# Performance work log

Measured on AMD Instinct MI355X. Metric: run time of the kernel, lower is better.

## Reference

```python
import jax, jax.numpy as jnp
import numpy as np

N = 2048          # target nodes
N_NODES = 2048    # neighbor pool
D_IN = 256
D_EDGE = 16
D_HID = 32
D_OUT = 256


def _mlp(h, w1, b1, w2, b2):
    # Linear -> Tanh -> Linear
    return jnp.tanh(h @ w1 + b1) @ w2 + b2


def setup_inputs() -> dict:
    key = jax.random.key(0)
    ks = jax.random.split(key, 20)
    s = 0.05
    inp = {
        "x": jax.random.normal(ks[0], (N, D_IN), jnp.float32),
        "neibs": jax.random.normal(ks[1], (N_NODES, D_IN), jnp.float32),
        "edge_emb": jax.random.normal(ks[2], (N * N_NODES, D_EDGE), jnp.float32),
        # multiplicative binary mask (float, as in original ws * mask)
        "mask": (jax.random.uniform(ks[3], (N, N_NODES)) < 0.7).astype(jnp.float32),
        "ax_w1": jax.random.normal(ks[4], (D_IN, D_HID), jnp.float32) * s,
        "ax_b1": jnp.zeros((D_HID,), jnp.float32),
        "ax_w2": jax.random.normal(ks[5], (D_HID, D_HID), jnp.float32) * s,
        "ax_b2": jnp.zeros((D_HID,), jnp.float32),
        "an_w1": jax.random.normal(ks[6], (D_IN, D_HID), jnp.float32) * s,
        "an_b1": jnp.zeros((D_HID,), jnp.float32),
        "an_w2": jax.random.normal(ks[7], (D_HID, D_HID), jnp.float32) * s,
        "an_b2": jnp.zeros((D_HID,), jnp.float32),
        "ae_w1": jax.random.normal(ks[8], (D_EDGE, D_HID), jnp.float32) * s,
        "ae_b1": jnp.zeros((D_HID,), jnp.float32),
        "ae_w2": jax.random.normal(ks[9], (D_HID, D_HID), jnp.float32) * s,
        "ae_b2": jnp.zeros((D_HID,), jnp.float32),
        "fcx_w": jax.random.normal(ks[10], (2 * D_IN, D_OUT), jnp.float32) * s,
        "fcx_b": jnp.zeros((D_OUT,), jnp.float32),
    }
    return inp


def reference(x, neibs, edge_emb, mask,
              ax_w1, ax_b1, ax_w2, ax_b2,
              an_w1, an_b1, an_w2, an_b2,
              ae_w1, ae_b1, ae_w2, ae_b2,
              fcx_w, fcx_b):
    x_att = _mlp(x, ax_w1, ax_b1, ax_w2, ax_b2)          # (N, H)
    neib_att = _mlp(neibs, an_w1, an_b1, an_w2, an_b2)   # (n_nodes, H)
    # edge attention is computed in the original forward but never used (dead code)
    _edge_att = _mlp(edge_emb, ae_w1, ae_b1, ae_w2, ae_b2)
    # multiplicative masking (NOT additive -inf), then softmax over neighbors
    ws = jnp.einsum('nh,mh->nm', x_att, neib_att) * mask  # (N, n_nodes)
    ws = jax.nn.softmax(ws, axis=1)
    agg_neib = jax.nn.sigmoid(ws @ neibs)                 # (N, D_IN)
    # concat_node=False path: concat -> fc_x -> sigmoid; dropout is identity (eval)
    out = jax.nn.sigmoid(jnp.concatenate([x, agg_neib], axis=1) @ fcx_w + fcx_b)
    return out
```

## Files before the change

kernel.cpp:

```cpp
#include <hip/hip_runtime.h>
#include <hip/hip_bf16.h>
#include <math.h>

#define NROWS 2048
#define DIN 256
#define DH 32
#define DOUT 256

typedef unsigned short ushort_t;
typedef unsigned int uint_t;
typedef __attribute__((ext_vector_type(8))) short short8;
typedef __attribute__((ext_vector_type(4))) float floatx4;

__device__ __forceinline__ float bf2f(uint_t u) {
    union { uint_t i; float f; } v; v.i = u << 16; return v.f;
}
__device__ __forceinline__ ushort_t f2bf(float f) {
    __hip_bfloat16 h = __float2bfloat16(f);
    union { __hip_bfloat16 h; ushort_t u; } v; v.h = h; return v.u;
}
__device__ __forceinline__ float sigm(float v) { return 1.0f / (1.0f + __expf(-v)); }

#define PSTR 2072
#define ASTR 536

__global__ __launch_bounds__(256) void prep_kernel(
    const float* __restrict__ x, const float* __restrict__ neibs,
    const float* __restrict__ ax_w1, const float* __restrict__ ax_b1,
    const float* __restrict__ ax_w2, const float* __restrict__ ax_b2,
    const float* __restrict__ an_w1, const float* __restrict__ an_b1,
    const float* __restrict__ an_w2, const float* __restrict__ an_b2,
    const float* __restrict__ fcx_w,
    float* __restrict__ x_att, ushort_t* __restrict__ n_att,
    short8* __restrict__ B_pack, short8* __restrict__ W_pack)
{
    const int t = threadIdx.x;
    const int b = blockIdx.x;

    __shared__ float srow[8][DIN];
    __shared__ float hbuf[8][DH];

    if (b < 512) {
        const bool is_x = b < 256;
        const int row0 = (is_x ? b : b - 256) * 8;
        const float* __restrict__ in = is_x ? x : neibs;
        const float* __restrict__ w1 = is_x ? ax_w1 : an_w1;
        const float* __restrict__ b1 = is_x ? ax_b1 : an_b1;
        const float* __restrict__ w2 = is_x ? ax_w2 : an_w2;
        const float* __restrict__ b2 = is_x ? ax_b2 : an_b2;

        const int r = t >> 5, c = t & 31;
        {
            const float4* in4 = (const float4*)(in + (row0 + r) * DIN);
            float4 a = in4[c * 2], bb = in4[c * 2 + 1];
            *(float4*)&srow[r][c * 8] = a;
            *(float4*)&srow[r][c * 8 + 4] = bb;
        }
        __syncthreads();

        float s = b1[c];
#pragma unroll 8
        for (int k = 0; k < DIN; ++k) s += srow[r][k] * w1[k * DH + c];
        s = tanhf(s);
        hbuf[r][c] = s;
        __syncthreads();

        float s2 = b2[c];
#pragma unroll
        for (int j = 0; j < DH; ++j) s2 += hbuf[r][j] * w2[j * DH + c];

        if (is_x) x_att[(row0 + r) * DH + c] = s2;
        else      n_att[(row0 + r) * DH + c] = f2bf(s2);
    } else if (b < 768) {
        const int g = (b - 512) * 256 + t;
        const int n = g & 15, q = (g >> 4) & 3, tt = (g >> 6) & 3, w = (g >> 8) & 3;
        const int s = g >> 10;
        const int ncol = w * 64 + tt * 16 + n;
        const int kb = 32 * s + 8 * q;
        short8 v;
#pragma unroll
        for (int j = 0; j < 8; ++j)
            v[j] = (short)f2bf(neibs[(size_t)(kb + j) * DIN + ncol]);
        B_pack[g] = v;
    } else {
        const int g = (b - 768) * 256 + t;
        const int n = g & 15, q = (g >> 4) & 3, tt = (g >> 6) & 3, w = (g >> 8) & 3;
        const int s = g >> 10;
        const int ncol = w * 64 + tt * 16 + n;
        const int kb = 32 * s + 8 * q;
        short8 v;
#pragma unroll
        for (int j = 0; j < 8; ++j)
            v[j] = (short)f2bf(fcx_w[(size_t)(kb + j) * DOUT + ncol]);
        W_pack[g] = v;
    }
}

__global__ __launch_bounds__(256) void attn_kernel(
    const float* __restrict__ x, const float* __restrict__ mask,
    const float* __restrict__ x_att, const ushort_t* __restrict__ n_att,
    const short8* __restrict__ B_pack, const short8* __restrict__ W_pack,
    const float* __restrict__ fcx_b, float* __restrict__ out)
{
    __shared__ __align__(16) ushort_t pTr[8 * PSTR];
    __shared__ __align__(16) ushort_t ATr[8 * ASTR];
    __shared__ float row_inv[8];

    const int t = threadIdx.x;
    const int n0 = blockIdx.x * 8;
    const int wv = t >> 6, lane = t & 63;

#pragma unroll
    for (int r = 0; r < 8; ++r)
        ATr[r * ASTR + t] = f2bf(x[(size_t)(n0 + r) * DIN + t]);

    const int r0 = 2 * wv, r1 = r0 + 1;
    float xa0[DH], xa1[DH];
#pragma unroll
    for (int h = 0; h < DH; ++h) {
        xa0[h] = x_att[(n0 + r0) * DH + h];
        xa1[h] = x_att[(n0 + r1) * DH + h];
    }
    float mx0 = -1e30f, mx1 = -1e30f;
    const uint4* na4 = (const uint4*)n_att;
    for (int it = 0; it < 32; ++it) {
        const int m = it * 64 + lane;
        float s0 = 0.f, s1 = 0.f;
#pragma unroll
        for (int qq = 0; qq < 4; ++qq) {
            uint4 v = na4[m * 4 + qq];
            uint_t wsw[4] = { v.x, v.y, v.z, v.w };
#pragma unroll
            for (int u = 0; u < 4; ++u) {
                const float f0 = bf2f(wsw[u] & 0xffffu);
                const float f1 = bf2f(wsw[u] >> 16);
                const int h = qq * 8 + u * 2;
                s0 += xa0[h] * f0;     s1 += xa1[h] * f0;
                s0 += xa0[h + 1] * f1; s1 += xa1[h + 1] * f1;
            }
        }
        s0 *= mask[(size_t)(n0 + r0) * NROWS + m];
        s1 *= mask[(size_t)(n0 + r1) * NROWS + m];
        mx0 = fmaxf(mx0, s0); mx1 = fmaxf(mx1, s1);
        pTr[r0 * PSTR + m] = f2bf(s0);
        pTr[r1 * PSTR + m] = f2bf(s1);
    }
#pragma unroll
    for (int off = 32; off >= 1; off >>= 1) {
        mx0 = fmaxf(mx0, __shfl_xor(mx0, off));
        mx1 = fmaxf(mx1, __shfl_xor(mx1, off));
    }
    float l0 = 0.f, l1 = 0.f;
    for (int it = 0; it < 32; ++it) {
        const int m = it * 64 + lane;
        const float e0 = __expf(bf2f(pTr[r0 * PSTR + m]) - mx0);
        const float e1 = __expf(bf2f(pTr[r1 * PSTR + m]) - mx1);
        l0 += e0; l1 += e1;
        pTr[r0 * PSTR + m] = f2bf(e0);
        pTr[r1 * PSTR + m] = f2bf(e1);
    }
#pragma unroll
    for (int off = 32; off >= 1; off >>= 1) {
        l0 += __shfl_xor(l0, off);
        l1 += __shfl_xor(l1, off);
    }
    if (lane == 0) { row_inv[r0] = 1.f / l0; row_inv[r1] = 1.f / l1; }
    __syncthreads();

    const int q = lane >> 4;
    const int ar = lane & 7;
    const char* aBase = (const char*)pTr + ar * (PSTR * 2) + q * 16;

    floatx4 acc[4];
#pragma unroll
    for (int tt = 0; tt < 4; ++tt) acc[tt] = (floatx4){0.f, 0.f, 0.f, 0.f};

    for (int s = 0; s < 64; ++s) {
        const short8 av = *(const short8*)(aBase + s * 64);
#pragma unroll
        for (int tt = 0; tt < 4; ++tt) {
            const int slab = (s * 4 + wv) * 4 + tt;
            const short8 bv = B_pack[slab * 64 + lane];
            acc[tt] = __builtin_amdgcn_mfma_f32_16x16x32_bf16(av, bv, acc[tt], 0, 0, 0);
        }
    }
    if (lane < 32) {
        const int col = lane & 15;
        const int rbase = (lane >> 4) * 4;
#pragma unroll
        for (int tt = 0; tt < 4; ++tt) {
            const int n = wv * 64 + tt * 16 + col;
#pragma unroll
            for (int rg = 0; rg < 4; ++rg) {
                const int row = rbase + rg;
                ATr[row * ASTR + 256 + n] = f2bf(sigm(acc[tt][rg] * row_inv[row]));
            }
        }
    }
    __syncthreads();

    floatx4 acc2[4];
#pragma unroll
    for (int tt = 0; tt < 4; ++tt) acc2[tt] = (floatx4){0.f, 0.f, 0.f, 0.f};

    const char* a2Base = (const char*)ATr + ar * (ASTR * 2) + q * 16;
    for (int s = 0; s < 16; ++s) {
        const short8 av = *(const short8*)(a2Base + s * 64);
#pragma unroll
        for (int tt = 0; tt < 4; ++tt) {
            const int slab = (s * 4 + wv) * 4 + tt;
            const short8 bv = W_pack[slab * 64 + lane];
            acc2[tt] = __builtin_amdgcn_mfma_f32_16x16x32_bf16(av, bv, acc2[tt], 0, 0, 0);
        }
    }
    if (lane < 32) {
        const int col = lane & 15;
        const int rbase = (lane >> 4) * 4;
#pragma unroll
        for (int tt = 0; tt < 4; ++tt) {
            const int n = wv * 64 + tt * 16 + col;
            const float bias = fcx_b[n];
#pragma unroll
            for (int rg = 0; rg < 4; ++rg) {
                const int row = rbase + rg;
                out[(size_t)(n0 + row) * DOUT + n] = sigm(acc2[tt][rg] + bias);
            }
        }
    }
}

extern "C" void kernel_launch(void* const* d_in, const int* in_sizes, int n_in,
                              void* d_out, int out_size, void* d_ws, size_t ws_size,
                              hipStream_t stream) {
    const float* x      = (const float*)d_in[0];
    const float* neibs  = (const float*)d_in[1];
    const float* mask   = (const float*)d_in[3];
    const float* ax_w1  = (const float*)d_in[4];
    const float* ax_b1  = (const float*)d_in[5];
    const float* ax_w2  = (const float*)d_in[6];
    const float* ax_b2  = (const float*)d_in[7];
    const float* an_w1  = (const float*)d_in[8];
    const float* an_b1  = (const float*)d_in[9];
    const float* an_w2  = (const float*)d_in[10];
    const float* an_b2  = (const float*)d_in[11];
    const float* fcx_w  = (const float*)d_in[16];
    const float* fcx_b  = (const float*)d_in[17];
    float* out = (float*)d_out;

    char* ws = (char*)d_ws;
    float*    x_att  = (float*)ws;
    ushort_t* n_att  = (ushort_t*)(ws + 262144);
    short8*   B_pack = (short8*)(ws + 393216);
    short8*   W_pack = (short8*)(ws + 1441792);

    prep_kernel<<<832, 256, 0, stream>>>(
        x, neibs, ax_w1, ax_b1, ax_w2, ax_b2,
        an_w1, an_b1, an_w2, an_b2, fcx_w,
        x_att, n_att, B_pack, W_pack);

    attn_kernel<<<256, 256, 0, stream>>>(
        x, mask, x_att, n_att, B_pack, W_pack, fcx_b, out);
}
```

Baseline: 411.0 us.

## Use MFMA for attention scores, split-K with 8 waves, LDS-tiled weight packing

The attention-score dot products move from scalar FMAs over bf16-unpacked vectors to MFMA 16x16x32 on prepacked bf16 x_att and n_att fragments. The attention kernel doubles to 512 threads (8 waves), splitting K across two wave groups for both GEMMs with an LDS reduction, and softmax becomes one wave per row with a register-held pass. Prep packing now stages neibs and fcx_w tiles in LDS for coalesced reads and uses fewer blocks. Costs are extra syncs and LDS reduction traffic, and x_att is now rounded to bf16, which lowers the precision of the scores.

Result: faster. 384.1 us (-6.5%).

```diff
diff --git a/kernel.cpp b/kernel.cpp
--- a/kernel.cpp
+++ b/kernel.cpp
@@ -21,8 +21,8 @@
 }
 __device__ __forceinline__ float sigm(float v) { return 1.0f / (1.0f + __expf(-v)); }
 
-#define PSTR 2072
-#define ASTR 536
+#define PSTR 2056
+#define ASTR 520
 
 __global__ __launch_bounds__(256) void prep_kernel(
     const float* __restrict__ x, const float* __restrict__ neibs,
@@ -31,16 +31,18 @@
     const float* __restrict__ an_w1, const float* __restrict__ an_b1,
     const float* __restrict__ an_w2, const float* __restrict__ an_b2,
     const float* __restrict__ fcx_w,
-    float* __restrict__ x_att, ushort_t* __restrict__ n_att,
+    ushort_t* __restrict__ x_attB, short8* __restrict__ n_attP,
     short8* __restrict__ B_pack, short8* __restrict__ W_pack)
 {
+    __shared__ float smem[32 * 256];
     const int t = threadIdx.x;
     const int b = blockIdx.x;
 
-    __shared__ float srow[8][DIN];
-    __shared__ float hbuf[8][DH];
-
     if (b < 512) {
+        float (*srow)[DIN] = (float (*)[DIN])smem;
+        float* hbuf = smem + 8 * DIN;
+        float* sbuf = smem + 8 * DIN + 8 * DH;
+
         const bool is_x = b < 256;
         const int row0 = (is_x ? b : b - 256) * 8;
         const float* __restrict__ in = is_x ? x : neibs;
@@ -51,7 +53,7 @@
 
         const int r = t >> 5, c = t & 31;
         {
-            const float4* in4 = (const float4*)(in + (row0 + r) * DIN);
+            const float4* in4 = (const float4*)(in + (size_t)(row0 + r) * DIN);
             float4 a = in4[c * 2], bb = in4[c * 2 + 1];
             *(float4*)&srow[r][c * 8] = a;
             *(float4*)&srow[r][c * 8 + 4] = bb;
@@ -62,43 +64,75 @@
 #pragma unroll 8
         for (int k = 0; k < DIN; ++k) s += srow[r][k] * w1[k * DH + c];
         s = tanhf(s);
-        hbuf[r][c] = s;
+        hbuf[r * DH + c] = s;
         __syncthreads();
 
         float s2 = b2[c];
 #pragma unroll
-        for (int j = 0; j < DH; ++j) s2 += hbuf[r][j] * w2[j * DH + c];
-
-        if (is_x) x_att[(row0 + r) * DH + c] = s2;
-        else      n_att[(row0 + r) * DH + c] = f2bf(s2);
-    } else if (b < 768) {
-        const int g = (b - 512) * 256 + t;
-        const int n = g & 15, q = (g >> 4) & 3, tt = (g >> 6) & 3, w = (g >> 8) & 3;
-        const int s = g >> 10;
-        const int ncol = w * 64 + tt * 16 + n;
-        const int kb = 32 * s + 8 * q;
-        short8 v;
-#pragma unroll
-        for (int j = 0; j < 8; ++j)
-            v[j] = (short)f2bf(neibs[(size_t)(kb + j) * DIN + ncol]);
-        B_pack[g] = v;
+        for (int j = 0; j < DH; ++j) s2 += hbuf[r * DH + j] * w2[j * DH + c];
+
+        if (is_x) {
+            x_attB[(size_t)(row0 + r) * DH + c] = f2bf(s2);
+        } else {
+            sbuf[r * DH + c] = s2;
+            __syncthreads();
+            if (t < 32) {
+                const int r2 = t >> 2, q = t & 3;
+                const int row = row0 + r2;
+                short8 v;
+#pragma unroll
+                for (int j = 0; j < 8; ++j) v[j] = (short)f2bf(sbuf[r2 * DH + q * 8 + j]);
+                n_attP[(row >> 4) * 64 + q * 16 + (row & 15)] = v;
+            }
+        }
+    } else if (b < 576) {
+        const int s = b - 512;
+        float* tile = smem;
+#pragma unroll
+        for (int i = 0; i < 8; ++i) {
+            const int e = i * 256 + t;
+            const int row = e >> 6, c4 = e & 63;
+            const float4 v = ((const float4*)neibs)[(size_t)(32 * s + row) * 64 + c4];
+            *(float4*)&tile[row * 256 + c4 * 4] = v;
+        }
+        __syncthreads();
+#pragma unroll
+        for (int i = 0; i < 4; ++i) {
+            const int G = i * 256 + t;
+            const int n = G & 15, q = (G >> 4) & 3, tt = (G >> 6) & 3, w = G >> 8;
+            const int col = w * 64 + tt * 16 + n;
+            short8 v;
+#pragma unroll
+            for (int j = 0; j < 8; ++j) v[j] = (short)f2bf(tile[(8 * q + j) * 256 + col]);
+            B_pack[s * 1024 + G] = v;
+        }
     } else {
-        const int g = (b - 768) * 256 + t;
-        const int n = g & 15, q = (g >> 4) & 3, tt = (g >> 6) & 3, w = (g >> 8) & 3;
-        const int s = g >> 10;
-        const int ncol = w * 64 + tt * 16 + n;
-        const int kb = 32 * s + 8 * q;
-        short8 v;
-#pragma unroll
-        for (int j = 0; j < 8; ++j)
-            v[j] = (short)f2bf(fcx_w[(size_t)(kb + j) * DOUT + ncol]);
-        W_pack[g] = v;
-    }
-}
-
-__global__ __launch_bounds__(256) void attn_kernel(
+        const int s = b - 576;
+        float* tile = smem;
+#pragma unroll
+        for (int i = 0; i < 8; ++i) {
+            const int e = i * 256 + t;
+            const int row = e >> 6, c4 = e & 63;
+            const float4 v = ((const float4*)fcx_w)[(size_t)(32 * s + row) * 64 + c4];
+            *(float4*)&tile[row * 256 + c4 * 4] = v;
+        }
+        __syncthreads();
+#pragma unroll
+        for (int i = 0; i < 4; ++i) {
+            const int G = i * 256 + t;
+            const int n = G & 15, q = (G >> 4) & 3, tt = (G >> 6) & 3, w = G >> 8;
+            const int col = w * 64 + tt * 16 + n;
+            short8 v;
+#pragma unroll
+            for (int j = 0; j < 8; ++j) v[j] = (short)f2bf(tile[(8 * q + j) * 256 + col]);
+            W_pack[s * 1024 + G] = v;
+        }
+    }
+}
+
+__global__ __launch_bounds__(512, 2) void attn_kernel(
     const float* __restrict__ x, const float* __restrict__ mask,
-    const float* __restrict__ x_att, const ushort_t* __restrict__ n_att,
+    const ushort_t* __restrict__ x_attB, const short8* __restrict__ n_attP,
     const short8* __restrict__ B_pack, const short8* __restrict__ W_pack,
     const float* __restrict__ fcx_b, float* __restrict__ out)
 {
@@ -108,122 +142,145 @@
 
     const int t = threadIdx.x;
     const int n0 = blockIdx.x * 8;
-    const int wv = t >> 6, lane = t & 63;
-
-#pragma unroll
-    for (int r = 0; r < 8; ++r)
-        ATr[r * ASTR + t] = f2bf(x[(size_t)(n0 + r) * DIN + t]);
-
-    const int r0 = 2 * wv, r1 = r0 + 1;
-    float xa0[DH], xa1[DH];
-#pragma unroll
-    for (int h = 0; h < DH; ++h) {
-        xa0[h] = x_att[(n0 + r0) * DH + h];
-        xa1[h] = x_att[(n0 + r1) * DH + h];
-    }
-    float mx0 = -1e30f, mx1 = -1e30f;
-    const uint4* na4 = (const uint4*)n_att;
-    for (int it = 0; it < 32; ++it) {
-        const int m = it * 64 + lane;
-        float s0 = 0.f, s1 = 0.f;
-#pragma unroll
-        for (int qq = 0; qq < 4; ++qq) {
-            uint4 v = na4[m * 4 + qq];
-            uint_t wsw[4] = { v.x, v.y, v.z, v.w };
-#pragma unroll
-            for (int u = 0; u < 4; ++u) {
-                const float f0 = bf2f(wsw[u] & 0xffffu);
-                const float f1 = bf2f(wsw[u] >> 16);
-                const int h = qq * 8 + u * 2;
-                s0 += xa0[h] * f0;     s1 += xa1[h] * f0;
-                s0 += xa0[h + 1] * f1; s1 += xa1[h + 1] * f1;
-            }
-        }
-        s0 *= mask[(size_t)(n0 + r0) * NROWS + m];
-        s1 *= mask[(size_t)(n0 + r1) * NROWS + m];
-        mx0 = fmaxf(mx0, s0); mx1 = fmaxf(mx1, s1);
-        pTr[r0 * PSTR + m] = f2bf(s0);
-        pTr[r1 * PSTR + m] = f2bf(s1);
-    }
-#pragma unroll
-    for (int off = 32; off >= 1; off >>= 1) {
-        mx0 = fmaxf(mx0, __shfl_xor(mx0, off));
-        mx1 = fmaxf(mx1, __shfl_xor(mx1, off));
-    }
-    float l0 = 0.f, l1 = 0.f;
-    for (int it = 0; it < 32; ++it) {
-        const int m = it * 64 + lane;
-        const float e0 = __expf(bf2f(pTr[r0 * PSTR + m]) - mx0);
-        const float e1 = __expf(bf2f(pTr[r1 * PSTR + m]) - mx1);
-        l0 += e0; l1 += e1;
-        pTr[r0 * PSTR + m] = f2bf(e0);
-        pTr[r1 * PSTR + m] = f2bf(e1);
-    }
-#pragma unroll
-    for (int off = 32; off >= 1; off >>= 1) {
-        l0 += __shfl_xor(l0, off);
-        l1 += __shfl_xor(l1, off);
-    }
-    if (lane == 0) { row_inv[r0] = 1.f / l0; row_inv[r1] = 1.f / l1; }
-    __syncthreads();
-
-    const int q = lane >> 4;
-    const int ar = lane & 7;
-    const char* aBase = (const char*)pTr + ar * (PSTR * 2) + q * 16;
-
-    floatx4 acc[4];
-#pragma unroll
-    for (int tt = 0; tt < 4; ++tt) acc[tt] = (floatx4){0.f, 0.f, 0.f, 0.f};
-
-    for (int s = 0; s < 64; ++s) {
-        const short8 av = *(const short8*)(aBase + s * 64);
-#pragma unroll
-        for (int tt = 0; tt < 4; ++tt) {
-            const int slab = (s * 4 + wv) * 4 + tt;
-            const short8 bv = B_pack[slab * 64 + lane];
-            acc[tt] = __builtin_amdgcn_mfma_f32_16x16x32_bf16(av, bv, acc[tt], 0, 0, 0);
-        }
-    }
-    if (lane < 32) {
-        const int col = lane & 15;
-        const int rbase = (lane >> 4) * 4;
-#pragma unroll
-        for (int tt = 0; tt < 4; ++tt) {
-            const int n = wv * 64 + tt * 16 + col;
+    const int w = t >> 6, lane = t & 63;
+    const int q = lane >> 4, nn = lane & 15;
+    const int arow = lane & 7;
+    const int rbase = (lane >> 4) * 4;
+
+#pragma unroll
+    for (int i = 0; i < 4; ++i) {
+        const int e = i * 512 + t;
+        const int r = e >> 8, k = e & 255;
+        ATr[r * ASTR + k] = f2bf(x[(size_t)(n0 + r) * DIN + k]);
+    }
+
+    const short8 av_s = *(const short8*)(x_attB + (size_t)(n0 + arow) * DH + q * 8);
+#pragma unroll 4
+    for (int i = 0; i < 16; ++i) {
+        const int tl = w * 16 + i;
+        const short8 bv = n_attP[tl * 64 + lane];
+        floatx4 c = __builtin_amdgcn_mfma_f32_16x16x32_bf16(
+            av_s, bv, (floatx4){0.f, 0.f, 0.f, 0.f}, 0, 0, 0);
+        if (lane < 32) {
+            const int m = tl * 16 + nn;
 #pragma unroll
             for (int rg = 0; rg < 4; ++rg) {
                 const int row = rbase + rg;
-                ATr[row * ASTR + 256 + n] = f2bf(sigm(acc[tt][rg] * row_inv[row]));
+                const float sv = c[rg] * mask[(size_t)(n0 + row) * NROWS + m];
+                pTr[row * PSTR + m] = f2bf(sv);
             }
         }
     }
     __syncthreads();
 
+    {
+        ushort_t* prow = pTr + w * PSTR;
+        uint_t raw[16];
+        float mx = -1e30f;
+#pragma unroll
+        for (int j = 0; j < 16; ++j) {
+            raw[j] = *(const uint_t*)(prow + j * 128 + 2 * lane);
+            mx = fmaxf(mx, fmaxf(bf2f(raw[j] & 0xffffu), bf2f(raw[j] >> 16)));
+        }
+#pragma unroll
+        for (int off = 32; off >= 1; off >>= 1) mx = fmaxf(mx, __shfl_xor(mx, off));
+        float sum = 0.f;
+#pragma unroll
+        for (int j = 0; j < 16; ++j) {
+            const float e0 = __expf(bf2f(raw[j] & 0xffffu) - mx);
+            const float e1 = __expf(bf2f(raw[j] >> 16) - mx);
+            sum += e0 + e1;
+            *(uint_t*)(prow + j * 128 + 2 * lane) =
+                (uint_t)f2bf(e0) | ((uint_t)f2bf(e1) << 16);
+        }
+#pragma unroll
+        for (int off = 32; off >= 1; off >>= 1) sum += __shfl_xor(sum, off);
+        if (lane == 0) row_inv[w] = 1.f / sum;
+    }
+    __syncthreads();
+
+    const int cq = w & 3, kh = w >> 2;
+    const char* aBase = (const char*)pTr + arow * (PSTR * 2);
+    floatx4 acc[4];
+#pragma unroll
+    for (int tt = 0; tt < 4; ++tt) acc[tt] = (floatx4){0.f, 0.f, 0.f, 0.f};
+
+#pragma unroll 4
+    for (int si = 0; si < 32; ++si) {
+        const int s = kh * 32 + si;
+        const short8 av = *(const short8*)(aBase + s * 64 + q * 16);
+#pragma unroll
+        for (int tt = 0; tt < 4; ++tt) {
+            const short8 bv = B_pack[(s * 16 + cq * 4 + tt) * 64 + lane];
+            acc[tt] = __builtin_amdgcn_mfma_f32_16x16x32_bf16(av, bv, acc[tt], 0, 0, 0);
+        }
+    }
+    __syncthreads();
+    float* red = (float*)pTr;
+    if (kh == 1) {
+#pragma unroll
+        for (int tt = 0; tt < 4; ++tt)
+            *(floatx4*)&red[((cq * 4 + tt) * 64 + lane) * 4] = acc[tt];
+    }
+    __syncthreads();
+    if (kh == 0) {
+#pragma unroll
+        for (int tt = 0; tt < 4; ++tt) {
+            const floatx4 rv = *(const floatx4*)&red[((cq * 4 + tt) * 64 + lane) * 4];
+            acc[tt] += rv;
+        }
+        if (lane < 32) {
+#pragma unroll
+            for (int tt = 0; tt < 4; ++tt) {
+                const int n = cq * 64 + tt * 16 + nn;
+#pragma unroll
+                for (int rg = 0; rg < 4; ++rg) {
+                    const int row = rbase + rg;
+                    ATr[row * ASTR + 256 + n] = f2bf(sigm(acc[tt][rg] * row_inv[row]));
+                }
+            }
+        }
+    }
+    __syncthreads();
+
+    const char* a2 = (const char*)ATr + arow * (ASTR * 2);
     floatx4 acc2[4];
 #pragma unroll
     for (int tt = 0; tt < 4; ++tt) acc2[tt] = (floatx4){0.f, 0.f, 0.f, 0.f};
 
-    const char* a2Base = (const char*)ATr + ar * (ASTR * 2) + q * 16;
-    for (int s = 0; s < 16; ++s) {
-        const short8 av = *(const short8*)(a2Base + s * 64);
+#pragma unroll
+    for (int si = 0; si < 8; ++si) {
+        const int s = kh * 8 + si;
+        const short8 av = *(const short8*)(a2 + s * 64 + q * 16);
 #pragma unroll
         for (int tt = 0; tt < 4; ++tt) {
-            const int slab = (s * 4 + wv) * 4 + tt;
-            const short8 bv = W_pack[slab * 64 + lane];
+            const short8 bv = W_pack[(s * 16 + cq * 4 + tt) * 64 + lane];
             acc2[tt] = __builtin_amdgcn_mfma_f32_16x16x32_bf16(av, bv, acc2[tt], 0, 0, 0);
         }
     }
-    if (lane < 32) {
-        const int col = lane & 15;
-        const int rbase = (lane >> 4) * 4;
+    __syncthreads();
+    if (kh == 1) {
+#pragma unroll
+        for (int tt = 0; tt < 4; ++tt)
+            *(floatx4*)&red[((cq * 4 + tt) * 64 + lane) * 4] = acc2[tt];
+    }
+    __syncthreads();
+    if (kh == 0) {
 #pragma unroll
         for (int tt = 0; tt < 4; ++tt) {
-            const int n = wv * 64 + tt * 16 + col;
-            const float bias = fcx_b[n];
-#pragma unroll
-            for (int rg = 0; rg < 4; ++rg) {
-                const int row = rbase + rg;
-                out[(size_t)(n0 + row) * DOUT + n] = sigm(acc2[tt][rg] + bias);
+            const floatx4 rv = *(const floatx4*)&red[((cq * 4 + tt) * 64 + lane) * 4];
+            acc2[tt] += rv;
+        }
+        if (lane < 32) {
+#pragma unroll
+            for (int tt = 0; tt < 4; ++tt) {
+                const int n = cq * 64 + tt * 16 + nn;
+                const float bias = fcx_b[n];
+#pragma unroll
+                for (int rg = 0; rg < 4; ++rg) {
+                    const int row = rbase + rg;
+                    out[(size_t)(n0 + row) * DOUT + n] = sigm(acc2[tt][rg] + bias);
+                }
             }
         }
     }
@@ -248,16 +305,16 @@
     float* out = (float*)d_out;
 
     char* ws = (char*)d_ws;
-    float*    x_att  = (float*)ws;
-    ushort_t* n_att  = (ushort_t*)(ws + 262144);
-    short8*   B_pack = (short8*)(ws + 393216);
-    short8*   W_pack = (short8*)(ws + 1441792);
-
-    prep_kernel<<<832, 256, 0, stream>>>(
+    ushort_t* x_attB = (ushort_t*)ws;
+    short8*   n_attP = (short8*)(ws + 131072);
+    short8*   B_pack = (short8*)(ws + 262144);
+    short8*   W_pack = (short8*)(ws + 1310720);
+
+    prep_kernel<<<592, 256, 0, stream>>>(
         x, neibs, ax_w1, ax_b1, ax_w2, ax_b2,
         an_w1, an_b1, an_w2, an_b2, fcx_w,
-        x_att, n_att, B_pack, W_pack);
-
-    attn_kernel<<<256, 256, 0, stream>>>(
-        x, mask, x_att, n_att, B_pack, W_pack, fcx_b, out);
-}
+        x_attB, n_attP, B_pack, W_pack);
+
+    attn_kernel<<<256, 512, 0, stream>>>(
+        x, mask, x_attB, n_attP, B_pack, W_pack, fcx_b, out);
+}
```
